# Performance work log

Hardware: AMD Instinct MI355X
Metric: run time of the kernel (lower is better)

## Reference

```python
import jax, jax.numpy as jnp
import numpy as np

B, H, W, D = 4, 64, 64, 384
M, P = 12, 9
DH = D // M             # 32 head dim
DFF = 3 * D             # 1152 FFN hidden
N = H * W               # 4096 queries (single level)


def setup_inputs():
    key = jax.random.key(0)
    ks = jax.random.split(key, 12)
    g = lambda k, s, sc=0.02: jax.random.normal(k, s, jnp.float32) * sc
    return {
        "x": jax.random.normal(ks[0], (B, D, H, W), jnp.float32),
        "qry_masks": jnp.zeros((B, H, W), jnp.float32),
        "so_w": g(ks[1], (M * P * 2, D)), "so_b": g(ks[2], (M * P * 2,)),
        "aw_w": g(ks[3], (M * P, D)), "aw_b": g(ks[4], (M * P,)),
        "vp_w": g(ks[5], (D, D)), "vp_b": jnp.zeros((D,), jnp.float32),
        "op_w": g(ks[6], (D, D)), "op_b": jnp.zeros((D,), jnp.float32),
        "ln1_g": jnp.ones((D,), jnp.float32), "ln1_b": jnp.zeros((D,), jnp.float32),
        "w1": g(ks[7], (DFF, D)), "w2": g(ks[8], (D, DFF)),
        "ln2_g": jnp.ones((D,), jnp.float32), "ln2_b": jnp.zeros((D,), jnp.float32),
        "level_embed": g(ks[9], (1, D), 1.0),
    }


def _layernorm(x, g, b, eps=1e-5):
    mu = x.mean(-1, keepdims=True)
    v = ((x - mu) ** 2).mean(-1, keepdims=True)
    return (x - mu) * jax.lax.rsqrt(v + eps) * g + b


def _sine_pos(mask):
    # mask: [B,H,W] bool. mmdet SinePositionalEncoding(num_feats=D//2, normalize=True)
    not_mask = (~mask).astype(jnp.float32)
    y = jnp.cumsum(not_mask, 1)
    x = jnp.cumsum(not_mask, 2)
    eps, scale = 1e-6, 2.0 * np.pi
    y = y / (y[:, -1:, :] + eps) * scale
    x = x / (x[:, :, -1:] + eps) * scale
    nf = D // 2
    dim_t = 10000.0 ** (2.0 * (jnp.arange(nf) // 2).astype(jnp.float32) / nf)
    px, py = x[..., None] / dim_t, y[..., None] / dim_t

    def interleave(p):
        return jnp.stack([jnp.sin(p[..., 0::2]), jnp.cos(p[..., 1::2])], -1).reshape(p.shape[:-1] + (nf,))

    return jnp.concatenate([interleave(py), interleave(px)], -1)  # [B,H,W,D]


def _bilinear_gather(v, px, py):
    # v: [B,M,HW,DH]; px,py: [B,M,NP] pixel coords (grid_sample align_corners=False, zero pad)
    x0 = jnp.floor(px); y0 = jnp.floor(py)
    lx, ly = px - x0, py - y0
    x0i, y0i = x0.astype(jnp.int32), y0.astype(jnp.int32)
    out = jnp.zeros(v.shape[:2] + (px.shape[-1], v.shape[-1]), v.dtype)
    for dx, dy, wgt in ((0, 0, (1 - lx) * (1 - ly)), (1, 0, lx * (1 - ly)),
                        (0, 1, (1 - lx) * ly), (1, 1, lx * ly)):
        xi, yi = x0i + dx, y0i + dy
        valid = ((xi >= 0) & (xi < W) & (yi >= 0) & (yi < H)).astype(v.dtype)
        idx = jnp.clip(yi, 0, H - 1) * W + jnp.clip(xi, 0, W - 1)
        g = jnp.take_along_axis(v, idx[..., None], axis=2)  # [B,M,NP,DH]
        out = out + (wgt * valid)[..., None] * g
    return out


def _msdeform_attn(q, value_in, ref, mask_flat,
                   so_w, so_b, aw_w, aw_b, vp_w, vp_b, op_w, op_b):
    value = value_in @ vp_w.T + vp_b                      # [B,N,D]
    value = jnp.where(mask_flat[..., None], 0.0, value)
    so = (q @ so_w.T + so_b).reshape(B, N, M, P, 2)       # single level
    aw = jax.nn.softmax((q @ aw_w.T + aw_b).reshape(B, N, M, P), axis=-1)
    norm = jnp.array([W, H], jnp.float32)
    loc = ref[:, :, None, None, :] + so / norm            # [B,N,M,P,2] in [0,1]
    v = value.reshape(B, N, M, DH).transpose(0, 2, 1, 3)  # [B,M,HW,DH]
    px = (loc[..., 0] * W - 0.5).transpose(0, 2, 1, 3).reshape(B, M, N * P)
    py = (loc[..., 1] * H - 0.5).transpose(0, 2, 1, 3).reshape(B, M, N * P)
    sampled = _bilinear_gather(v, px, py).reshape(B, M, N, P, DH)
    out = jnp.einsum('bmnpd,bnmp->bnmd', sampled, aw).reshape(B, N, D)
    return out @ op_w.T + op_b


def reference(x, qry_masks, so_w, so_b, aw_w, aw_b, vp_w, vp_b, op_w, op_b,
              ln1_g, ln1_b, w1, w2, ln2_g, ln2_b, level_embed):
    mask = (qry_masks == 255.0)                           # [B,H,W] bool
    pos = _sine_pos(mask).reshape(B, N, D) + level_embed[0]
    src = x.reshape(B, D, N).transpose(0, 2, 1)           # [B,N,D]
    mask_flat = mask.reshape(B, N)
    gy, gx = jnp.meshgrid((jnp.arange(H, dtype=jnp.float32) + 0.5) / H,
                          (jnp.arange(W, dtype=jnp.float32) + 0.5) / W, indexing='ij')
    ref = jnp.stack([gx.reshape(-1), gy.reshape(-1)], -1)[None]  # [1,N,2] (x,y)
    q = src
    attn = _msdeform_attn(q + pos, q, ref, mask_flat,
                          so_w, so_b, aw_w, aw_b, vp_w, vp_b, op_w, op_b)
    q = _layernorm(q + attn, ln1_g, ln1_b)
    q = _layernorm(q + jax.nn.relu(q @ w1.T) @ w2.T, ln2_g, ln2_b)
    return q.transpose(0, 2, 1).reshape(B, D, H, W)
```

## Files before the change

### kernel.cpp

```cpp
#include <hip/hip_runtime.h>
#include <math.h>

#define Bc   4
#define Hc   64
#define Wc   64
#define Dc   384
#define Nc   4096
#define Mc   12
#define Pc   9
#define DHc  32
#define DFFc 1152
#define BNc  (Bc*Nc)

typedef __attribute__((ext_vector_type(8))) short short8;
typedef __attribute__((ext_vector_type(4))) float floatx4;

__device__ __forceinline__ ushort f2bf(float f) {
    union { float f; unsigned u; } v; v.f = f;
    unsigned r = v.u + 0x7fffu + ((v.u >> 16) & 1u);
    return (ushort)(r >> 16);
}

__device__ __forceinline__ void gload_lds16(const void* g, void* l) {
    __builtin_amdgcn_global_load_lds(
        (const __attribute__((address_space(1))) void*)(uintptr_t)g,
        (__attribute__((address_space(3))) void*)(uintptr_t)l,
        16, 0, 0);
}

#define SOW_N  82944
#define AWW_N  41472
#define VPW_N  147456
#define OPW_N  147456
#define W1_N   442368
#define W2_N   442368
#define WTOT   1304064

__global__ void init_kernel(const float* __restrict__ so_w,
                            const float* __restrict__ aw_w,
                            const float* __restrict__ vp_w,
                            const float* __restrict__ op_w,
                            const float* __restrict__ w1,
                            const float* __restrict__ w2,
                            const float* __restrict__ so_b,
                            const float* __restrict__ aw_b,
                            const float* __restrict__ qmask,
                            ushort* __restrict__ out,
                            float* __restrict__ bias_out,
                            float* __restrict__ cum_y,
                            float* __restrict__ cum_x) {
    int i = blockIdx.x * 256 + threadIdx.x;
    if (i < WTOT) {
        float v;
        int j = i;
        if (j < SOW_N) v = so_w[j];
        else if ((j -= SOW_N) < AWW_N) v = aw_w[j];
        else if ((j -= AWW_N) < VPW_N) v = vp_w[j];
        else if ((j -= VPW_N) < OPW_N) v = op_w[j];
        else if ((j -= OPW_N) < W1_N)  v = w1[j];
        else { j -= W1_N; v = w2[j]; }
        out[i] = f2bf(v);
        return;
    }
    int j = i - WTOT;
    if (j < 384) {
        bias_out[j] = (j < 216) ? so_b[j] : (j < 324 ? aw_b[j - 216] : 0.f);
        return;
    }
    int t = j - 384;
    if (t < Bc * Wc) {
        int b = t / Wc, w = t % Wc;
        float run = 0.f;
        for (int h = 0; h < Hc; ++h) {
            run += (qmask[(b * Hc + h) * Wc + w] == 255.0f) ? 0.f : 1.f;
            cum_y[(b * Hc + h) * Wc + w] = run;
        }
    } else if (t < Bc * Wc + Bc * Hc) {
        int t2 = t - Bc * Wc;
        int b = t2 / Hc, h = t2 % Hc;
        float run = 0.f;
        for (int w = 0; w < Wc; ++w) {
            run += (qmask[(b * Hc + h) * Wc + w] == 255.0f) ? 0.f : 1.f;
            cum_x[(b * Hc + h) * Wc + w] = run;
        }
    }
}

__global__ void transpose_pos_kernel(const float* __restrict__ x,
                                     const float* __restrict__ cum_y,
                                     const float* __restrict__ cum_x,
                                     const float* __restrict__ level_embed,
                                     float* __restrict__ src_f,
                                     ushort* __restrict__ src_bf,
                                     ushort* __restrict__ qpos_bf) {
    __shared__ float tile[32][33];
    int b  = blockIdx.z;
    int n0 = blockIdx.x * 32, d0 = blockIdx.y * 32;
    int tx = threadIdx.x, ty = threadIdx.y;
    tile[ty][tx] = x[((size_t)b * Dc + (d0 + ty)) * Nc + (n0 + tx)];
    __syncthreads();
    int n = n0 + ty, d = d0 + tx;
    float v = tile[tx][ty];
    size_t oi = ((size_t)b * Nc + n) * Dc + d;
    src_f[oi]  = v;
    src_bf[oi] = f2bf(v);
    int h = n >> 6, w = n & 63;
    const float TWO_PI = 6.28318530717958647692f;
    float vy = cum_y[(b * Hc + h) * Wc + w] /
               (cum_y[(b * Hc + (Hc - 1)) * Wc + w] + 1e-6f) * TWO_PI;
    float vx = cum_x[(b * Hc + h) * Wc + w] /
               (cum_x[(b * Hc + h) * Wc + (Wc - 1)] + 1e-6f) * TWO_PI;
    int   i  = (d < 192) ? d : d - 192;
    float vv = (d < 192) ? vy : vx;
    float e   = (float)(i >> 1) * (2.0f / 192.0f);
    float idt = exp2f(e * -13.28771237954945f);
    float ang = vv * idt;
    float pe  = (i & 1) ? __cosf(ang) : __sinf(ang);
    qpos_bf[oi] = f2bf(v + pe + level_embed[d]);
}

template <int KT>
__global__ __launch_bounds__(256) void gemm_v8_kernel(
        const ushort* __restrict__ A, const ushort* __restrict__ Wt,
        const float* __restrict__ bias,
        float* __restrict__ Cf, ushort* __restrict__ Cb,
        int Nout, int relu, const float* __restrict__ qmask) {
    constexpr int NCH = KT / 32;
    __shared__ ushort As[2][128 * 32];
    __shared__ ushort Bs[2][128 * 32];
    const int tid  = threadIdx.x;
    const int m0   = blockIdx.x * 128;
    const int n0   = blockIdx.y * 128;
    const int lane = tid & 63;
    const int wv   = tid >> 6;
    const int wr   = (wv >> 1) * 64;
    const int wc   = (wv & 1) * 64;
    const int quad = lane >> 4;
    const int lrow = lane & 15;
    const int srow = wv * 32 + (lane >> 2);
    const int scol = (lane & 3) * 8;

    floatx4 acc[4][4];
    #pragma unroll
    for (int i = 0; i < 4; ++i)
        #pragma unroll
        for (int j = 0; j < 4; ++j)
            acc[i][j] = (floatx4)(0.f);

    #pragma unroll
    for (int s = 0; s < 2; ++s) {
        gload_lds16(A  + (size_t)(m0 + srow + s * 16) * KT + scol,
                    &As[0][wv * 1024 + s * 512]);
        gload_lds16(Wt + (size_t)(n0 + srow + s * 16) * KT + scol,
                    &Bs[0][wv * 1024 + s * 512]);
    }

    for (int c = 0; c < NCH; ++c) {
        const int cur = c & 1;
        __syncthreads();
        if (c + 1 < NCH) {
            const int k0 = (c + 1) * 32;
            #pragma unroll
            for (int s = 0; s < 2; ++s) {
                gload_lds16(A  + (size_t)(m0 + srow + s * 16) * KT + k0 + scol,
                            &As[cur ^ 1][wv * 1024 + s * 512]);
                gload_lds16(Wt + (size_t)(n0 + srow + s * 16) * KT + k0 + scol,
                            &Bs[cur ^ 1][wv * 1024 + s * 512]);
            }
        }
        short8 afr[4], bfr[4];
        #pragma unroll
        for (int i = 0; i < 4; ++i)
            afr[i] = *(const short8*)(&As[cur][(wr + i * 16 + lrow) * 32 + quad * 8]);
        #pragma unroll
        for (int j = 0; j < 4; ++j)
            bfr[j] = *(const short8*)(&Bs[cur][(wc + j * 16 + lrow) * 32 + quad * 8]);
        #pragma unroll
        for (int i = 0; i < 4; ++i)
            #pragma unroll
            for (int j = 0; j < 4; ++j)
                acc[i][j] = __builtin_amdgcn_mfma_f32_16x16x32_bf16(
                    afr[i], bfr[j], acc[i][j], 0, 0, 0);
    }

    float mz[4][4];
    #pragma unroll
    for (int i = 0; i < 4; ++i)
        #pragma unroll
        for (int r = 0; r < 4; ++r) {
            int row = m0 + wr + i * 16 + quad * 4 + r;
            mz[i][r] = (qmask && qmask[row] == 255.0f) ? 0.f : 1.f;
        }

    #pragma unroll
    for (int i = 0; i < 4; ++i) {
        #pragma unroll
        for (int j = 0; j < 4; ++j) {
            int col = n0 + wc + j * 16 + lrow;
            if (col >= Nout) continue;
            float bsv = bias ? bias[col] : 0.f;
            #pragma unroll
            for (int r = 0; r < 4; ++r) {
                int row = m0 + wr + i * 16 + quad * 4 + r;
                float v = acc[i][j][r] + bsv;
                if (relu) v = fmaxf(v, 0.f);
                v *= mz[i][r];
                if (Cf) Cf[(size_t)row * Nout + col] = v;
                if (Cb) Cb[(size_t)row * Nout + col] = f2bf(v);
            }
        }
    }
}

__global__ __launch_bounds__(256) void deform_attn_kernel(
        const ushort* __restrict__ value_bf, const float* __restrict__ soaw,
        ushort* __restrict__ out) {
    int gid = blockIdx.x * 64 + (threadIdx.x >> 2);
    int l4  = threadIdx.x & 3;
    int m  = gid % Mc;
    int bn = gid / Mc;
    int b  = bn >> 12;
    int n  = bn & 4095;
    int h  = n >> 6, w = n & 63;
    const float* sop = soaw + (size_t)bn * 384 + m * 18;
    const float* lgt = soaw + (size_t)bn * 384 + 216 + m * Pc;
    float awv[Pc];
    float mx = lgt[0];
    #pragma unroll
    for (int i = 1; i < Pc; ++i) mx = fmaxf(mx, lgt[i]);
    float ssum = 0.f;
    #pragma unroll
    for (int i = 0; i < Pc; ++i) { awv[i] = __expf(lgt[i] - mx); ssum += awv[i]; }
    float sinv = 1.f / ssum;
    const ushort* vb = value_bf + ((size_t)b * Nc) * Dc + m * DHc + l4 * 8;
    float acc[8] = {0.f, 0.f, 0.f, 0.f, 0.f, 0.f, 0.f, 0.f};
    #pragma unroll
    for (int p = 0; p < Pc; ++p) {
        float2 so2 = *(const float2*)(sop + p * 2);
        float px = (float)w + so2.x;
        float py = (float)h + so2.y;
        float x0f = floorf(px), y0f = floorf(py);
        float lx = px - x0f, ly = py - y0f;
        int x0 = (int)x0f, y0 = (int)y0f;
        int x1 = x0 + 1,  y1 = y0 + 1;
        float a = awv[p] * sinv;
        float w00 = (1.f - lx) * (1.f - ly) * a;
        float w01 = lx * (1.f - ly) * a;
        float w10 = (1.f - lx) * ly * a;
        float w11 = lx * ly * a;
        bool bx0 = (unsigned)x0 < 64u, bx1 = (unsigned)x1 < 64u;
        bool by0 = (unsigned)y0 < 64u, by1 = (unsigned)y1 < 64u;
        w00 = (bx0 && by0) ? w00 : 0.f;
        w01 = (bx1 && by0) ? w01 : 0.f;
        w10 = (bx0 && by1) ? w10 : 0.f;
        w11 = (bx1 && by1) ? w11 : 0.f;
        int cx0 = min(max(x0, 0), 63), cx1 = min(max(x1, 0), 63);
        int cy0 = min(max(y0, 0), 63), cy1 = min(max(y1, 0), 63);
        uint4 q00 = *(const uint4*)(vb + (size_t)(cy0 * 64 + cx0) * Dc);
        uint4 q01 = *(const uint4*)(vb + (size_t)(cy0 * 64 + cx1) * Dc);
        uint4 q10 = *(const uint4*)(vb + (size_t)(cy1 * 64 + cx0) * Dc);
        uint4 q11 = *(const uint4*)(vb + (size_t)(cy1 * 64 + cx1) * Dc);
        union { unsigned u; float f; } t;
        #define ACC2(word, wg, k)                                   \
            t.u = (word) << 16;         acc[k]     += (wg) * t.f;   \
            t.u = (word) & 0xffff0000u; acc[k + 1] += (wg) * t.f;
        #define ACC8(q, wg) \
            ACC2((q).x, wg, 0) ACC2((q).y, wg, 2) ACC2((q).z, wg, 4) ACC2((q).w, wg, 6)
        ACC8(q00, w00) ACC8(q01, w01) ACC8(q10, w10) ACC8(q11, w11)
        #undef ACC8
        #undef ACC2
    }
    short8 o;
    #pragma unroll
    for (int k = 0; k < 8; ++k) o[k] = (short)f2bf(acc[k]);
    *(short8*)(out + (size_t)bn * Dc + m * DHc + l4 * 8) = o;
}

__global__ __launch_bounds__(128) void ln_residual_kernel(
        const float* a, const float* r,
        const float* g, const float* beta,
        float* out, ushort* outb) {
    int row = blockIdx.x;
    int tid = threadIdx.x;
    float4 v = make_float4(0.f, 0.f, 0.f, 0.f);
    if (tid < 96) {
        float4 av = ((const float4*)(a + (size_t)row * Dc))[tid];
        float4 rv = ((const float4*)(r + (size_t)row * Dc))[tid];
        v.x = av.x + rv.x; v.y = av.y + rv.y;
        v.z = av.z + rv.z; v.w = av.w + rv.w;
    }
    float s1 = v.x + v.y + v.z + v.w;
    float s2 = v.x * v.x + v.y * v.y + v.z * v.z + v.w * v.w;
    __shared__ float sh1[128], sh2[128];
    sh1[tid] = s1; sh2[tid] = s2;
    __syncthreads();
    for (int off = 64; off > 0; off >>= 1) {
        if (tid < off) { sh1[tid] += sh1[tid + off]; sh2[tid] += sh2[tid + off]; }
        __syncthreads();
    }
    float mu  = sh1[0] * (1.0f / Dc);
    float var = sh2[0] * (1.0f / Dc) - mu * mu;
    float rs  = rsqrtf(var + 1e-5f);
    if (tid < 96) {
        float4 gv = ((const float4*)g)[tid];
        float4 bv = ((const float4*)beta)[tid];
        float4 o;
        o.x = (v.x - mu) * rs * gv.x + bv.x;
        o.y = (v.y - mu) * rs * gv.y + bv.y;
        o.z = (v.z - mu) * rs * gv.z + bv.z;
        o.w = (v.w - mu) * rs * gv.w + bv.w;
        ((float4*)(out + (size_t)row * Dc))[tid] = o;
        if (outb) {
            ushort4 ob;
            ob.x = f2bf(o.x); ob.y = f2bf(o.y);
            ob.z = f2bf(o.z); ob.w = f2bf(o.w);
            ((ushort4*)(outb + (size_t)row * Dc))[tid] = ob;
        }
    }
}

__global__ void transpose_out_kernel(const float* __restrict__ src,
                                     float* __restrict__ out) {
    __shared__ float tile[32][33];
    int b  = blockIdx.z;
    int n0 = blockIdx.x * 32, d0 = blockIdx.y * 32;
    int tx = threadIdx.x, ty = threadIdx.y;
    tile[ty][tx] = src[((size_t)b * Nc + (n0 + ty)) * Dc + (d0 + tx)];
    __syncthreads();
    out[((size_t)b * Dc + (d0 + ty)) * Nc + (n0 + tx)] = tile[tx][ty];
}

extern "C" void kernel_launch(void* const* d_in, const int* in_sizes, int n_in,
                              void* d_out, int out_size, void* d_ws, size_t ws_size,
                              hipStream_t stream) {
    (void)in_sizes; (void)n_in; (void)out_size; (void)ws_size;
    const float* x      = (const float*)d_in[0];
    const float* qmask  = (const float*)d_in[1];
    const float* so_w   = (const float*)d_in[2];
    const float* so_b   = (const float*)d_in[3];
    const float* aw_w   = (const float*)d_in[4];
    const float* aw_b   = (const float*)d_in[5];
    const float* vp_w   = (const float*)d_in[6];
    const float* vp_b   = (const float*)d_in[7];
    const float* op_w   = (const float*)d_in[8];
    const float* op_b   = (const float*)d_in[9];
    const float* ln1_g  = (const float*)d_in[10];
    const float* ln1_b  = (const float*)d_in[11];
    const float* w1     = (const float*)d_in[12];
    const float* w2     = (const float*)d_in[13];
    const float* ln2_g  = (const float*)d_in[14];
    const float* ln2_b  = (const float*)d_in[15];
    const float* lvl    = (const float*)d_in[16];
    float* out = (float*)d_out;

    float*  ws       = (float*)d_ws;
    float*  src_f    = ws;
    float*  proj_f   = src_f + 6291456;
    ushort* src_bf   = (ushort*)(proj_f + 6291456);
    ushort* qpos_bf  = src_bf + 6291456;
    ushort* value_bf = qpos_bf + 6291456;
    ushort* hbuf_bf  = value_bf + 6291456;
    float*  soaw_f   = (float*)hbuf_bf;
    ushort* wbuf     = hbuf_bf + 18874368;
    float*  soaw_bias= (float*)(wbuf + 1304064);
    float*  cum_y    = soaw_bias + 384;
    float*  cum_x    = cum_y + 16384;

    const ushort* soaw_wb = wbuf;
    const ushort* vp_wb = soaw_wb + SOW_N + AWW_N;
    const ushort* op_wb = vp_wb + VPW_N;
    const ushort* w1_b  = op_wb + OPW_N;
    const ushort* w2_b  = w1_b + W1_N;

    init_kernel<<<(WTOT + 384 + 512 + 255) / 256, 256, 0, stream>>>(
        so_w, aw_w, vp_w, op_w, w1, w2, so_b, aw_b, qmask,
        wbuf, soaw_bias, cum_y, cum_x);
    transpose_pos_kernel<<<dim3(Nc / 32, Dc / 32, Bc), dim3(32, 32), 0, stream>>>(
        x, cum_y, cum_x, lvl, src_f, src_bf, qpos_bf);
    gemm_v8_kernel<384><<<dim3(BNc / 128, 3), 256, 0, stream>>>(
        qpos_bf, soaw_wb, soaw_bias, soaw_f, nullptr, 384, 0, nullptr);
    gemm_v8_kernel<384><<<dim3(BNc / 128, 3), 256, 0, stream>>>(
        src_bf, vp_wb, vp_b, nullptr, value_bf, Dc, 0, qmask);
    deform_attn_kernel<<<(BNc * Mc) / 64, 256, 0, stream>>>(
        value_bf, soaw_f, qpos_bf);
    gemm_v8_kernel<384><<<dim3(BNc / 128, 3), 256, 0, stream>>>(
        qpos_bf, op_wb, op_b, proj_f, nullptr, Dc, 0, nullptr);
    ln_residual_kernel<<<BNc, 128, 0, stream>>>(
        src_f, proj_f, ln1_g, ln1_b, src_f, qpos_bf);
    gemm_v8_kernel<384><<<dim3(BNc / 128, 9), 256, 0, stream>>>(
        qpos_bf, w1_b, nullptr, nullptr, hbuf_bf, DFFc, 1, nullptr);
    gemm_v8_kernel<1152><<<dim3(BNc / 128, 3), 256, 0, stream>>>(
        hbuf_bf, w2_b, nullptr, proj_f, nullptr, Dc, 0, nullptr);
    ln_residual_kernel<<<BNc, 128, 0, stream>>>(
        src_f, proj_f, ln2_g, ln2_b, src_f, nullptr);
    transpose_out_kernel<<<dim3(Nc / 32, Dc / 32, Bc), dim3(32, 32), 0, stream>>>(
        src_f, out);
}
```

Measured before the change: 299.2 us.

## Merge projection GEMMs, fuse LN2 with output transpose, shrink intermediates to bf16

The sampling-offset/weight GEMM and the value-projection GEMM now run as one launch selected by blockIdx.z. LN2 is fused with the final NCHW transpose, which removes a kernel and an fp32 round trip. GEMM outputs feeding the layer norms are stored in bf16 and the fp32 copy of src is dropped, with the residual read back from bf16. Deformable-attention blocks are remapped so that consecutive blocks are spread out. Together these cut memory traffic and launch count, at the cost of lower residual precision, and the LN2 output store is strided per thread.

Result: faster. 271.9 us (-9.1%).

```diff
diff --git a/kernel.cpp b/kernel.cpp
--- a/kernel.cpp
+++ b/kernel.cpp
@@ -19,6 +19,9 @@
     union { float f; unsigned u; } v; v.f = f;
     unsigned r = v.u + 0x7fffu + ((v.u >> 16) & 1u);
     return (ushort)(r >> 16);
+}
+__device__ __forceinline__ float bf2f(ushort u) {
+    union { unsigned u; float f; } v; v.u = (unsigned)u << 16; return v.f;
 }
 
 __device__ __forceinline__ void gload_lds16(const void* g, void* l) {
@@ -90,7 +93,6 @@
                                      const float* __restrict__ cum_y,
                                      const float* __restrict__ cum_x,
                                      const float* __restrict__ level_embed,
-                                     float* __restrict__ src_f,
                                      ushort* __restrict__ src_bf,
                                      ushort* __restrict__ qpos_bf) {
     __shared__ float tile[32][33];
@@ -102,7 +104,6 @@
     int n = n0 + ty, d = d0 + tx;
     float v = tile[tx][ty];
     size_t oi = ((size_t)b * Nc + n) * Dc + d;
-    src_f[oi]  = v;
     src_bf[oi] = f2bf(v);
     int h = n >> 6, w = n & 63;
     const float TWO_PI = 6.28318530717958647692f;
@@ -120,14 +121,13 @@
 }
 
 template <int KT>
-__global__ __launch_bounds__(256) void gemm_v8_kernel(
+__device__ __forceinline__ void gemm_core(
         const ushort* __restrict__ A, const ushort* __restrict__ Wt,
         const float* __restrict__ bias,
         float* __restrict__ Cf, ushort* __restrict__ Cb,
-        int Nout, int relu, const float* __restrict__ qmask) {
+        int Nout, int relu, const float* __restrict__ qmask,
+        ushort* As, ushort* Bs) {
     constexpr int NCH = KT / 32;
-    __shared__ ushort As[2][128 * 32];
-    __shared__ ushort Bs[2][128 * 32];
     const int tid  = threadIdx.x;
     const int m0   = blockIdx.x * 128;
     const int n0   = blockIdx.y * 128;
@@ -150,9 +150,9 @@
     #pragma unroll
     for (int s = 0; s < 2; ++s) {
         gload_lds16(A  + (size_t)(m0 + srow + s * 16) * KT + scol,
-                    &As[0][wv * 1024 + s * 512]);
+                    As + wv * 1024 + s * 512);
         gload_lds16(Wt + (size_t)(n0 + srow + s * 16) * KT + scol,
-                    &Bs[0][wv * 1024 + s * 512]);
+                    Bs + wv * 1024 + s * 512);
     }
 
     for (int c = 0; c < NCH; ++c) {
@@ -163,18 +163,20 @@
             #pragma unroll
             for (int s = 0; s < 2; ++s) {
                 gload_lds16(A  + (size_t)(m0 + srow + s * 16) * KT + k0 + scol,
-                            &As[cur ^ 1][wv * 1024 + s * 512]);
+                            As + (cur ^ 1) * 4096 + wv * 1024 + s * 512);
                 gload_lds16(Wt + (size_t)(n0 + srow + s * 16) * KT + k0 + scol,
-                            &Bs[cur ^ 1][wv * 1024 + s * 512]);
+                            Bs + (cur ^ 1) * 4096 + wv * 1024 + s * 512);
             }
         }
         short8 afr[4], bfr[4];
         #pragma unroll
         for (int i = 0; i < 4; ++i)
-            afr[i] = *(const short8*)(&As[cur][(wr + i * 16 + lrow) * 32 + quad * 8]);
+            afr[i] = *(const short8*)(As + cur * 4096 +
+                                      (wr + i * 16 + lrow) * 32 + quad * 8);
         #pragma unroll
         for (int j = 0; j < 4; ++j)
-            bfr[j] = *(const short8*)(&Bs[cur][(wc + j * 16 + lrow) * 32 + quad * 8]);
+            bfr[j] = *(const short8*)(Bs + cur * 4096 +
+                                      (wc + j * 16 + lrow) * 32 + quad * 8);
         #pragma unroll
         for (int i = 0; i < 4; ++i)
             #pragma unroll
@@ -212,10 +214,37 @@
     }
 }
 
+template <int KT>
+__global__ __launch_bounds__(256) void gemm_single_kernel(
+        const ushort* __restrict__ A, const ushort* __restrict__ Wt,
+        const float* __restrict__ bias,
+        float* __restrict__ Cf, ushort* __restrict__ Cb,
+        int Nout, int relu, const float* __restrict__ qmask) {
+    __shared__ ushort As[2 * 128 * 32];
+    __shared__ ushort Bs[2 * 128 * 32];
+    gemm_core<KT>(A, Wt, bias, Cf, Cb, Nout, relu, qmask, As, Bs);
+}
+
+__global__ __launch_bounds__(256) void gemm_dual_kernel(
+        const ushort* __restrict__ A0, const ushort* __restrict__ W0,
+        const float* __restrict__ b0, float* __restrict__ Cf0,
+        const ushort* __restrict__ A1, const ushort* __restrict__ W1,
+        const float* __restrict__ b1, ushort* __restrict__ Cb1,
+        const float* __restrict__ qmask) {
+    __shared__ ushort As[2 * 128 * 32];
+    __shared__ ushort Bs[2 * 128 * 32];
+    if (blockIdx.z == 0)
+        gemm_core<384>(A0, W0, b0, Cf0, nullptr, 384, 0, nullptr, As, Bs);
+    else
+        gemm_core<384>(A1, W1, b1, nullptr, Cb1, 384, 0, qmask, As, Bs);
+}
+
 __global__ __launch_bounds__(256) void deform_attn_kernel(
         const ushort* __restrict__ value_bf, const float* __restrict__ soaw,
         ushort* __restrict__ out) {
-    int gid = blockIdx.x * 64 + (threadIdx.x >> 2);
+    int bid = blockIdx.x;
+    int gb  = (bid & 7) * 384 + (bid >> 3);
+    int gid = gb * 64 + (threadIdx.x >> 2);
     int l4  = threadIdx.x & 3;
     int m  = gid % Mc;
     int bn = gid / Mc;
@@ -276,18 +305,18 @@
     *(short8*)(out + (size_t)bn * Dc + m * DHc + l4 * 8) = o;
 }
 
-__global__ __launch_bounds__(128) void ln_residual_kernel(
-        const float* a, const float* r,
-        const float* g, const float* beta,
-        float* out, ushort* outb) {
+__global__ __launch_bounds__(128) void ln1_kernel(
+        const ushort* __restrict__ a, const ushort* __restrict__ r,
+        const float* __restrict__ g, const float* __restrict__ beta,
+        float* __restrict__ outf, ushort* __restrict__ outb) {
     int row = blockIdx.x;
     int tid = threadIdx.x;
     float4 v = make_float4(0.f, 0.f, 0.f, 0.f);
     if (tid < 96) {
-        float4 av = ((const float4*)(a + (size_t)row * Dc))[tid];
-        float4 rv = ((const float4*)(r + (size_t)row * Dc))[tid];
-        v.x = av.x + rv.x; v.y = av.y + rv.y;
-        v.z = av.z + rv.z; v.w = av.w + rv.w;
+        ushort4 av = ((const ushort4*)(a + (size_t)row * Dc))[tid];
+        ushort4 rv = ((const ushort4*)(r + (size_t)row * Dc))[tid];
+        v.x = bf2f(av.x) + bf2f(rv.x); v.y = bf2f(av.y) + bf2f(rv.y);
+        v.z = bf2f(av.z) + bf2f(rv.z); v.w = bf2f(av.w) + bf2f(rv.w);
     }
     float s1 = v.x + v.y + v.z + v.w;
     float s2 = v.x * v.x + v.y * v.y + v.z * v.z + v.w * v.w;
@@ -309,25 +338,61 @@
         o.y = (v.y - mu) * rs * gv.y + bv.y;
         o.z = (v.z - mu) * rs * gv.z + bv.z;
         o.w = (v.w - mu) * rs * gv.w + bv.w;
-        ((float4*)(out + (size_t)row * Dc))[tid] = o;
-        if (outb) {
-            ushort4 ob;
-            ob.x = f2bf(o.x); ob.y = f2bf(o.y);
-            ob.z = f2bf(o.z); ob.w = f2bf(o.w);
-            ((ushort4*)(outb + (size_t)row * Dc))[tid] = ob;
-        }
-    }
-}
-
-__global__ void transpose_out_kernel(const float* __restrict__ src,
-                                     float* __restrict__ out) {
-    __shared__ float tile[32][33];
-    int b  = blockIdx.z;
-    int n0 = blockIdx.x * 32, d0 = blockIdx.y * 32;
-    int tx = threadIdx.x, ty = threadIdx.y;
-    tile[ty][tx] = src[((size_t)b * Nc + (n0 + ty)) * Dc + (d0 + tx)];
+        ((float4*)(outf + (size_t)row * Dc))[tid] = o;
+        ushort4 ob;
+        ob.x = f2bf(o.x); ob.y = f2bf(o.y);
+        ob.z = f2bf(o.z); ob.w = f2bf(o.w);
+        ((ushort4*)(outb + (size_t)row * Dc))[tid] = ob;
+    }
+}
+
+__global__ __launch_bounds__(256) void ln2_transpose_kernel(
+        const float* __restrict__ q1, const ushort* __restrict__ r,
+        const float* __restrict__ g, const float* __restrict__ beta,
+        float* __restrict__ out) {
+    __shared__ float tile[32 * 388];
+    __shared__ float ps1[256], ps2[256];
+    __shared__ float mu_[32], rs_[32];
+    const int b  = blockIdx.y;
+    const int n0 = blockIdx.x * 32;
+    const int tid = threadIdx.x;
+    const int rr  = tid >> 3;
+    const int s8  = tid & 7;
+    const size_t row = (size_t)b * Nc + n0 + rr;
+    float s1 = 0.f, s2 = 0.f;
+    #pragma unroll
+    for (int i = 0; i < 12; ++i) {
+        int c = s8 * 48 + i * 4;
+        float4  av = *(const float4*)(q1 + row * Dc + c);
+        ushort4 rv = *(const ushort4*)(r + row * Dc + c);
+        float4 t;
+        t.x = av.x + bf2f(rv.x); t.y = av.y + bf2f(rv.y);
+        t.z = av.z + bf2f(rv.z); t.w = av.w + bf2f(rv.w);
+        *(float4*)&tile[rr * 388 + c] = t;
+        s1 += t.x + t.y + t.z + t.w;
+        s2 += t.x * t.x + t.y * t.y + t.z * t.z + t.w * t.w;
+    }
+    ps1[tid] = s1; ps2[tid] = s2;
     __syncthreads();
-    out[((size_t)b * Dc + (d0 + ty)) * Nc + (n0 + tx)] = tile[tx][ty];
+    if (tid < 32) {
+        float a1 = 0.f, a2 = 0.f;
+        #pragma unroll
+        for (int k = 0; k < 8; ++k) { a1 += ps1[tid * 8 + k]; a2 += ps2[tid * 8 + k]; }
+        float mu = a1 * (1.0f / Dc);
+        float var = a2 * (1.0f / Dc) - mu * mu;
+        mu_[tid] = mu;
+        rs_[tid] = rsqrtf(var + 1e-5f);
+    }
+    __syncthreads();
+    const int dg = tid >> 5;
+    const int nn = tid & 31;
+    float mu = mu_[nn], rs = rs_[nn];
+    #pragma unroll
+    for (int j = 0; j < 48; ++j) {
+        int d = dg * 48 + j;
+        float val = (tile[nn * 388 + d] - mu) * rs * g[d] + beta[d];
+        out[((size_t)b * Dc + d) * Nc + n0 + nn] = val;
+    }
 }
 
 extern "C" void kernel_launch(void* const* d_in, const int* in_sizes, int n_in,
@@ -354,12 +419,12 @@
     float* out = (float*)d_out;
 
     float*  ws       = (float*)d_ws;
-    float*  src_f    = ws;
-    float*  proj_f   = src_f + 6291456;
-    ushort* src_bf   = (ushort*)(proj_f + 6291456);
+    float*  q1_f     = ws;
+    ushort* src_bf   = (ushort*)(q1_f + 6291456);
     ushort* qpos_bf  = src_bf + 6291456;
     ushort* value_bf = qpos_bf + 6291456;
-    ushort* hbuf_bf  = value_bf + 6291456;
+    ushort* proj_bf  = value_bf + 6291456;
+    ushort* hbuf_bf  = proj_bf + 6291456;
     float*  soaw_f   = (float*)hbuf_bf;
     ushort* wbuf     = hbuf_bf + 18874368;
     float*  soaw_bias= (float*)(wbuf + 1304064);
@@ -376,23 +441,20 @@
         so_w, aw_w, vp_w, op_w, w1, w2, so_b, aw_b, qmask,
         wbuf, soaw_bias, cum_y, cum_x);
     transpose_pos_kernel<<<dim3(Nc / 32, Dc / 32, Bc), dim3(32, 32), 0, stream>>>(
-        x, cum_y, cum_x, lvl, src_f, src_bf, qpos_bf);
-    gemm_v8_kernel<384><<<dim3(BNc / 128, 3), 256, 0, stream>>>(
-        qpos_bf, soaw_wb, soaw_bias, soaw_f, nullptr, 384, 0, nullptr);
-    gemm_v8_kernel<384><<<dim3(BNc / 128, 3), 256, 0, stream>>>(
-        src_bf, vp_wb, vp_b, nullptr, value_bf, Dc, 0, qmask);
+        x, cum_y, cum_x, lvl, src_bf, qpos_bf);
+    gemm_dual_kernel<<<dim3(BNc / 128, 3, 2), 256, 0, stream>>>(
+        qpos_bf, soaw_wb, soaw_bias, soaw_f,
+        src_bf, vp_wb, vp_b, value_bf, qmask);
     deform_attn_kernel<<<(BNc * Mc) / 64, 256, 0, stream>>>(
         value_bf, soaw_f, qpos_bf);
-    gemm_v8_kernel<384><<<dim3(BNc / 128, 3), 256, 0, stream>>>(
-        qpos_bf, op_wb, op_b, proj_f, nullptr, Dc, 0, nullptr);
-    ln_residual_kernel<<<BNc, 128, 0, stream>>>(
-        src_f, proj_f, ln1_g, ln1_b, src_f, qpos_bf);
-    gemm_v8_kernel<384><<<dim3(BNc / 128, 9), 256, 0, stream>>>(
+    gemm_single_kernel<384><<<dim3(BNc / 128, 3), 256, 0, stream>>>(
+        qpos_bf, op_wb, op_b, nullptr, proj_bf, Dc, 0, nullptr);
+    ln1_kernel<<<BNc, 128, 0, stream>>>(
+        src_bf, proj_bf, ln1_g, ln1_b, q1_f, qpos_bf);
+    gemm_single_kernel<384><<<dim3(BNc / 128, 9), 256, 0, stream>>>(
         qpos_bf, w1_b, nullptr, nullptr, hbuf_bf, DFFc, 1, nullptr);
-    gemm_v8_kernel<1152><<<dim3(BNc / 128, 3), 256, 0, stream>>>(
-        hbuf_bf, w2_b, nullptr, proj_f, nullptr, Dc, 0, nullptr);
-    ln_residual_kernel<<<BNc, 128, 0, stream>>>(
-        src_f, proj_f, ln2_g, ln2_b, src_f, nullptr);
-    transpose_out_kernel<<<dim3(Nc / 32, Dc / 32, Bc), dim3(32, 32), 0, stream>>>(
-        src_f, out);
-}
+    gemm_single_kernel<1152><<<dim3(BNc / 128, 3), 256, 0, stream>>>(
+        hbuf_bf, w2_b, nullptr, nullptr, proj_bf, Dc, 0, nullptr);
+    ln2_transpose_kernel<<<dim3(Nc / 32, Bc), 256, 0, stream>>>(
+        q1_f, proj_bf, ln2_g, ln2_b, out);
+}
```
